# Performance work log

Measured on AMD Instinct MI355X. Metric: run time of the kernel, lower is better.

Reference implementation:

```python
import jax, jax.numpy as jnp
import numpy as np

N_NODES = 50000
N_EDGES = 600000
N_FEAT = 256
N_HID = 128
N_CLASS = 64
HEADS = 8
LEAKY_SLOPE = 0.2


def setup_inputs() -> dict:
    key = jax.random.key(0)
    ks = jax.random.split(key, 12)
    D0 = N_HID // HEADS  # 16 per-head dim, layer 0
    x = jax.random.normal(ks[0], (N_NODES, N_FEAT), dtype=jnp.float32)
    edge_index = jax.random.randint(ks[1], (2, N_EDGES), 0, N_NODES, dtype=jnp.int64)
    s0 = 1.0 / np.sqrt(N_FEAT)
    s1 = 1.0 / np.sqrt(N_HID)
    return {
        "x": x,
        "edge_index": edge_index,
        "W0": jax.random.normal(ks[2], (N_FEAT, HEADS * D0), dtype=jnp.float32) * s0,
        "a_src0": jax.random.normal(ks[3], (HEADS, D0), dtype=jnp.float32) * s0,
        "a_dst0": jax.random.normal(ks[4], (HEADS, D0), dtype=jnp.float32) * s0,
        "b0": jnp.zeros((HEADS * D0,), dtype=jnp.float32),
        "W1": jax.random.normal(ks[5], (N_HID, HEADS * N_CLASS), dtype=jnp.float32) * s1,
        "a_src1": jax.random.normal(ks[6], (HEADS, N_CLASS), dtype=jnp.float32) * s1,
        "a_dst1": jax.random.normal(ks[7], (HEADS, N_CLASS), dtype=jnp.float32) * s1,
        "b1": jnp.zeros((N_CLASS,), dtype=jnp.float32),
    }


def gat_conv(x, src, dst, W, a_s, a_d, b, concat, num_nodes):
    H, D = a_s.shape
    h = (x @ W).reshape(-1, H, D)                    # [N, H, D]
    alpha_s = jnp.einsum('nhd,hd->nh', h, a_s)       # [N, H]
    alpha_d = jnp.einsum('nhd,hd->nh', h, a_d)       # [N, H]
    e = jax.nn.leaky_relu(alpha_s[src] + alpha_d[dst], LEAKY_SLOPE)  # [E, H]
    # numerically stable edge-softmax grouped by destination node
    m = jax.ops.segment_max(e, dst, num_segments=num_nodes)
    m = jnp.where(jnp.isfinite(m), m, 0.0)           # nodes with no in-edges
    ex = jnp.exp(e - m[dst])
    denom = jax.ops.segment_sum(ex, dst, num_segments=num_nodes)
    alpha = ex / (denom[dst] + 1e-16)                # [E, H]
    msg = h[src] * alpha[:, :, None]                 # [E, H, D]
    out = jax.ops.segment_sum(msg, dst, num_segments=num_nodes)  # [N, H, D]
    if concat:
        out = out.reshape(num_nodes, H * D)
    else:
        out = out.mean(axis=1)
    return out + b


def reference(x, edge_index, W0, a_src0, a_dst0, b0, W1, a_src1, a_dst1, b1):
    src, dst = edge_index[0], edge_index[1]
    h = gat_conv(x, src, dst, W0, a_src0, a_dst0, b0, True, N_NODES)
    h = jax.nn.elu(h)  # eval mode: dropout is identity
    h = gat_conv(h, src, dst, W1, a_src1, a_dst1, b1, False, N_NODES)
    return jax.nn.log_softmax(h, axis=-1)
```

## Files before the change

### kernel.cpp

```cpp
#include <hip/hip_runtime.h>
#include <hip/hip_bf16.h>
#include <math.h>

#define NN 50000
#define NE 600000
#define NF 256
#define NHID 128
#define HEADS 8
#define D0 16
#define NCLS 64
#define NB1 196

#define PK0 (9 * 8 * 64 * 8)
#define PK1 (4 * 32 * 64 * 8)
#define PKA (4 * 64 * 8)
#define PREPN (PK0 + PK1 + PKA)

typedef __attribute__((ext_vector_type(8))) short short8;
typedef __attribute__((ext_vector_type(4))) float floatx4;

__device__ __forceinline__ float bf16lo(uint v) { return __uint_as_float((v & 0xffffu) << 16); }
__device__ __forceinline__ float bf16hi(uint v) { return __uint_as_float(v & 0xffff0000u); }
__device__ __forceinline__ uint packbf16(float a, float b) {
    return (uint)__bfloat16_as_ushort(__float2bfloat16(a)) |
           ((uint)__bfloat16_as_ushort(__float2bfloat16(b)) << 16);
}
__device__ __forceinline__ short f2bf(float v) {
    return (short)__bfloat16_as_ushort(__float2bfloat16(v));
}
__device__ __forceinline__ float bf16tof(short v) {
    return __uint_as_float(((uint)(ushort)v) << 16);
}


__global__ void scan1_kernel(const int* __restrict__ deg, int* __restrict__ rs,
                             int* __restrict__ bsum) {
    __shared__ int sh[256];
    int tid = threadIdx.x;
    int i = blockIdx.x * 256 + tid;
    int v = (i < NN) ? deg[i] : 0;
    sh[tid] = v;
    __syncthreads();
    for (int off = 1; off < 256; off <<= 1) {
        int t = (tid >= off) ? sh[tid - off] : 0;
        __syncthreads();
        sh[tid] += t;
        __syncthreads();
    }
    if (i < NN) rs[i] = sh[tid] - v;
    if (tid == 255) bsum[blockIdx.x] = sh[255];
}

__global__ void scan2_kernel(const int* __restrict__ bsum, int* __restrict__ bsumx) {
    __shared__ int sh[256];
    int tid = threadIdx.x;
    int v = (tid < NB1) ? bsum[tid] : 0;
    sh[tid] = v;
    __syncthreads();
    for (int off = 1; off < 256; off <<= 1) {
        int t = (tid >= off) ? sh[tid - off] : 0;
        __syncthreads();
        sh[tid] += t;
        __syncthreads();
    }
    if (tid < NB1) bsumx[tid] = sh[tid] - v;
}

__global__ void scan3_kernel(int* __restrict__ rs, const int* __restrict__ bsumx) {
    int i = blockIdx.x * 256 + threadIdx.x;
    if (i < NN) rs[i] += bsumx[i >> 8];
}

__global__ void scatter_kernel(const int* __restrict__ ei, const int* __restrict__ rs,
                               int* __restrict__ cnt2, int* __restrict__ csr) {
    int e = blockIdx.x * 256 + threadIdx.x;
    if (e >= NE) return;
    int s = ei[e], d = ei[NE + e];
    int pos = rs[d] + atomicAdd(&cnt2[d], 1);
    csr[pos] = s;
}


__global__ void fused_prep_kernel(const int* __restrict__ ei, int* __restrict__ deg,
                                  const float* __restrict__ W0, const float* __restrict__ aS0,
                                  const float* __restrict__ aD0, const float* __restrict__ W1,
                                  const float* __restrict__ aS1, const float* __restrict__ aD1,
                                  short* __restrict__ Bp0, short* __restrict__ Bp1,
                                  short* __restrict__ wA1b) {
    int e = blockIdx.x * 256 + threadIdx.x;
    if (e < NE) {
        atomicAdd(&deg[ei[NE + e]], 1);
        return;
    }
    int tid = e - NE;
    if (tid < PK0) {
        int j = tid & 7, l = (tid >> 3) & 63, ks = (tid >> 9) & 7, t = tid >> 12;
        int k = ks * 32 + (l >> 4) * 8 + j;
        float v;
        if (t < 8) {
            int c = t * 16 + (l & 15);
            v = W0[(size_t)k * 128 + c];
        } else {
            int jj = l & 15;
            int hh = jj & 7;
            const float* av = (jj < 8) ? aS0 : aD0;
            float sum = 0.f;
            for (int dd = 0; dd < D0; ++dd)
                sum += W0[(size_t)k * 128 + hh * D0 + dd] * av[hh * D0 + dd];
            v = sum;
        }
        Bp0[tid] = f2bf(v);
    } else if (tid < PK0 + PK1) {
        int t2 = tid - PK0;
        int j = t2 & 7, l = (t2 >> 3) & 63, ks = (t2 >> 9) & 31, t = t2 >> 14;
        int kk = ks * 32 + (l >> 4) * 8 + j;
        int c = t * 16 + (l & 15);
        Bp1[t2] = f2bf(W1[(size_t)(kk & 127) * 512 + (kk >> 7) * 64 + c] * 0.125f);
    } else if (tid < PREPN) {
        int t3 = tid - PK0 - PK1;
        int j = t3 & 7, l = (t3 >> 3) & 63, ks = t3 >> 9;
        int k = ks * 32 + (l >> 4) * 8 + j;
        int c = l & 15;
        int h = c & 7;
        const float* av = (c < 8) ? aS1 : aD1;
        float sum = 0.f;
        for (int d2 = 0; d2 < NCLS; ++d2)
            sum += W1[(size_t)k * 512 + h * NCLS + d2] * av[h * NCLS + d2];
        wA1b[t3] = f2bf(sum);
    }
}


__global__ __launch_bounds__(256) void gemm0_mfma(const float* __restrict__ x,
                                                  const short* __restrict__ Bp,
                                                  ushort* __restrict__ h0b,
                                                  float* __restrict__ as0,
                                                  float* __restrict__ ad0) {
    int lane = threadIdx.x & 63, wave = threadIdx.x >> 6;
    int rg = wave >> 1, cg = wave & 1;
    int q = lane >> 4, c16 = lane & 15;
    int row0 = blockIdx.x * 32 + rg * 16;
    int arow = row0 + c16;
    if (arow > NN - 1) arow = NN - 1;
    const float* ap = x + (size_t)arow * NF + q * 8;
    floatx4 acc[5] = {};
#pragma unroll
    for (int ks = 0; ks < 8; ++ks) {
        float4 va = *(const float4*)(ap + ks * 32);
        float4 vb = *(const float4*)(ap + ks * 32 + 4);
        short8 af;
        af[0] = f2bf(va.x); af[1] = f2bf(va.y); af[2] = f2bf(va.z); af[3] = f2bf(va.w);
        af[4] = f2bf(vb.x); af[5] = f2bf(vb.y); af[6] = f2bf(vb.z); af[7] = f2bf(vb.w);
#pragma unroll
        for (int tt = 0; tt < 4; ++tt) {
            int t = cg * 4 + tt;
            short8 bf = *(const short8*)(Bp + (((size_t)t * 8 + ks) * 64 + lane) * 8);
            acc[tt] = __builtin_amdgcn_mfma_f32_16x16x32_bf16(af, bf, acc[tt], 0, 0, 0);
        }
        if (cg) {
            short8 bf = *(const short8*)(Bp + (((size_t)8 * 8 + ks) * 64 + lane) * 8);
            acc[4] = __builtin_amdgcn_mfma_f32_16x16x32_bf16(af, bf, acc[4], 0, 0, 0);
        }
    }
#pragma unroll
    for (int r = 0; r < 4; ++r) {
        int grow = row0 + q * 4 + r;
        if (grow >= NN) continue;
#pragma unroll
        for (int tt = 0; tt < 4; ++tt)
            h0b[(size_t)grow * NHID + cg * 64 + tt * 16 + c16] =
                (ushort)f2bf(acc[tt][r]);
        if (cg) {
            float v = acc[4][r];
            if (c16 < 8) as0[grow * 8 + c16] = v;
            else         ad0[grow * 8 + (c16 - 8)] = v;
        }
    }
}

__global__ __launch_bounds__(256) void alpha1_mfma(const ushort* __restrict__ x1b,
                                                   const short* __restrict__ wA1b,
                                                   float* __restrict__ as1,
                                                   float* __restrict__ ad1) {
    int lane = threadIdx.x & 63, wave = threadIdx.x >> 6;
    int q = lane >> 4, c16 = lane & 15;
    int row0 = blockIdx.x * 64 + wave * 16;
    int arow = row0 + c16;
    if (arow > NN - 1) arow = NN - 1;
    const short* ap = (const short*)x1b + (size_t)arow * NHID + q * 8;
    floatx4 acc = {};
#pragma unroll
    for (int ks = 0; ks < 4; ++ks) {
        short8 af = *(const short8*)(ap + ks * 32);
        short8 bf = *(const short8*)(wA1b + (((size_t)ks) * 64 + lane) * 8);
        acc = __builtin_amdgcn_mfma_f32_16x16x32_bf16(af, bf, acc, 0, 0, 0);
    }
#pragma unroll
    for (int r = 0; r < 4; ++r) {
        int grow = row0 + q * 4 + r;
        if (grow >= NN) continue;
        float v = acc[r];
        if (c16 < 8) as1[grow * 8 + c16] = v;
        else         ad1[grow * 8 + (c16 - 8)] = v;
    }
}


__global__ __launch_bounds__(256) void fused_edge0(
    const int* __restrict__ rs, const int* __restrict__ deg, const int* __restrict__ csr,
    const ushort* __restrict__ h0b, const float* __restrict__ as0, const float* __restrict__ ad0,
    const float* __restrict__ b0, ushort* __restrict__ x1b) {
    int d = (blockIdx.x * 256 + threadIdx.x) >> 6;
    int lane = threadIdx.x & 63;
    if (d >= NN) return;
    int row = rs[d], dg = deg[d];
    int hl = lane & 7, g = lane >> 3;
    int hp = lane >> 3;
    float adv = ad0[d * 8 + hl];
    float den = 0.f;
    float2 acc = {0.f, 0.f};
    for (int base = 0; base < dg; base += 16) {
        int i0 = base + g, i1 = base + 8 + g;
        int s0 = (i0 < dg) ? csr[row + i0] : 0;
        int s1 = (i1 < dg) ? csr[row + i1] : 0;
        float ev0 = as0[s0 * 8 + hl] + adv;
        ev0 = ev0 > 0.f ? ev0 : 0.2f * ev0;
        float p0 = (i0 < dg) ? __expf(ev0) : 0.f;
        float ev1 = as0[s1 * 8 + hl] + adv;
        ev1 = ev1 > 0.f ? ev1 : 0.2f * ev1;
        float p1 = (i1 < dg) ? __expf(ev1) : 0.f;
        den += p0 + p1;
        uint vbuf[16];
#pragma unroll
        for (int g2 = 0; g2 < 8; ++g2) {
            int sg = __builtin_amdgcn_readlane(s0, g2 * 8);
            vbuf[g2] = *(const uint*)(h0b + (size_t)sg * NHID + 2 * lane);
        }
#pragma unroll
        for (int g2 = 0; g2 < 8; ++g2) {
            int sg = __builtin_amdgcn_readlane(s1, g2 * 8);
            vbuf[8 + g2] = *(const uint*)(h0b + (size_t)sg * NHID + 2 * lane);
        }
#pragma unroll
        for (int g2 = 0; g2 < 8; ++g2) {
            float ph = __shfl(p0, g2 * 8 + hp);
            acc.x += bf16lo(vbuf[g2]) * ph;
            acc.y += bf16hi(vbuf[g2]) * ph;
        }
#pragma unroll
        for (int g2 = 0; g2 < 8; ++g2) {
            float ph = __shfl(p1, g2 * 8 + hp);
            acc.x += bf16lo(vbuf[8 + g2]) * ph;
            acc.y += bf16hi(vbuf[8 + g2]) * ph;
        }
    }
    den += __shfl_xor(den, 8);
    den += __shfl_xor(den, 16);
    den += __shfl_xor(den, 32);
    float dh = __shfl(den, hp);
    float inv = 1.f / (dh + 1e-16f);
    float2 bb = ((const float2*)b0)[lane];
    float o0 = acc.x * inv + bb.x;
    float o1 = acc.y * inv + bb.y;
    o0 = o0 > 0.f ? o0 : expf(o0) - 1.f;
    o1 = o1 > 0.f ? o1 : expf(o1) - 1.f;
    *(uint*)(x1b + (size_t)d * NHID + 2 * lane) = packbf16(o0, o1);
}

__global__ __launch_bounds__(256) void fused_edge1(
    const int* __restrict__ rs, const int* __restrict__ deg, const int* __restrict__ csr,
    const ushort* __restrict__ x1b, const float* __restrict__ as1, const float* __restrict__ ad1,
    const short* __restrict__ Bp1, const float* __restrict__ b1, float* __restrict__ out) {
    __shared__ ushort aggNsh[8][1032];
    __shared__ float Csh[4][8][64];
    int wave = threadIdx.x >> 6;
    int lane = threadIdx.x & 63;
    int gw = blockIdx.x * 4 + wave;
    int dA = 2 * gw;
    int dB = dA + 1;
    int q = lane >> 4, c16 = lane & 15, h7 = lane & 7;
    int d_l = (lane >= 32) ? dB : dA;
    int row_l = rs[d_l], dg_l = deg[d_l];
    bool V = ((lane & 8) == 0) == (lane < 32);
    float adv = ad1[d_l * 8 + h7];
    int dgA = __shfl(dg_l, 0);
    int dgB = __shfl(dg_l, 32);
    int dgmax = dgA > dgB ? dgA : dgB;
    float den = 0.f;
    floatx4 acc[8] = {};
    for (int base = 0; base < dgmax; base += 16) {
        short8 af;
        int sarr[8];
#pragma unroll
        for (int j = 0; j < 8; ++j) {
            int idx = base + (q & 1) * 8 + j;
            int s = 0;
            if (idx < dg_l) s = csr[row_l + idx];
            sarr[j] = s;
            float ev = as1[s * 8 + h7] + adv;
            ev = ev > 0.f ? ev : 0.2f * ev;
            float p = __expf(ev);
            p = (idx < dg_l && V) ? p : 0.f;
            short pb = f2bf(p);
            af[j] = pb;
            den += bf16tof(pb);
        }
#pragma unroll
        for (int t = 0; t < 8; ++t) {
            short8 bv;
#pragma unroll
            for (int j = 0; j < 8; ++j)
                bv[j] = (short)x1b[(size_t)sarr[j] * NHID + t * 16 + c16];
            acc[t] = __builtin_amdgcn_mfma_f32_16x16x32_bf16(af, bv, acc[t], 0, 0, 0);
        }
    }
    den += __shfl_xor(den, 8);
    den += __shfl_xor(den, 16);
    int hbase = (q & 1) * 4;
    int lrow = wave * 2 + (lane >> 5);
#pragma unroll
    for (int r = 0; r < 4; ++r) {
        int hh = hbase + r;
        float dh = __shfl(den, (lane & 32) + hh);
        float inv = 1.f / (dh + 1e-16f);
#pragma unroll
        for (int t = 0; t < 8; ++t)
            aggNsh[lrow][hh * 128 + t * 16 + c16] = (ushort)f2bf(acc[t][r] * inv);
    }
    __syncthreads();
    {
        floatx4 acc2[4] = {};
        const short* abase = (const short*)&aggNsh[c16 & 7][0];
        int ks0 = wave * 8;
#pragma unroll
        for (int kk = 0; kk < 8; ++kk) {
            int ks = ks0 + kk;
            short8 af2 = *(const short8*)(abase + ks * 32 + q * 8);
#pragma unroll
            for (int t = 0; t < 4; ++t) {
                short8 bf = *(const short8*)(Bp1 + (((size_t)t * 32 + ks) * 64 + lane) * 8);
                acc2[t] = __builtin_amdgcn_mfma_f32_16x16x32_bf16(af2, bf, acc2[t], 0, 0, 0);
            }
        }
        if (q < 2) {
#pragma unroll
            for (int r = 0; r < 4; ++r)
#pragma unroll
                for (int t = 0; t < 4; ++t)
                    Csh[wave][q * 4 + r][t * 16 + c16] = acc2[t][r];
        }
    }
    __syncthreads();
    float z0 = 0.f, z1 = 0.f;
#pragma unroll
    for (int w2 = 0; w2 < 4; ++w2) {
        z0 += Csh[w2][wave * 2][lane];
        z1 += Csh[w2][wave * 2 + 1][lane];
    }
    float bb = b1[lane];
    z0 += bb;
    z1 += bb;
    float mx0 = z0, mx1 = z1;
#pragma unroll
    for (int x = 1; x < 64; x <<= 1) {
        mx0 = fmaxf(mx0, __shfl_xor(mx0, x));
        mx1 = fmaxf(mx1, __shfl_xor(mx1, x));
    }
    float s0 = expf(z0 - mx0), s1 = expf(z1 - mx1);
#pragma unroll
    for (int x = 1; x < 64; x <<= 1) {
        s0 += __shfl_xor(s0, x);
        s1 += __shfl_xor(s1, x);
    }
    float lse0 = mx0 + logf(s0);
    float lse1 = mx1 + logf(s1);
    out[(size_t)dA * NCLS + lane] = z0 - lse0;
    out[(size_t)dB * NCLS + lane] = z1 - lse1;
}


extern "C" void kernel_launch(void* const* d_in, const int* in_sizes, int n_in,
                              void* d_out, int out_size, void* d_ws, size_t ws_size,
                              hipStream_t stream) {
    const float* x   = (const float*)d_in[0];
    const int*   ei  = (const int*)d_in[1];
    const float* W0  = (const float*)d_in[2];
    const float* aS0 = (const float*)d_in[3];
    const float* aD0 = (const float*)d_in[4];
    const float* b0  = (const float*)d_in[5];
    const float* W1  = (const float*)d_in[6];
    const float* aS1 = (const float*)d_in[7];
    const float* aD1 = (const float*)d_in[8];
    const float* b1  = (const float*)d_in[9];
    float* out = (float*)d_out;

    char* ws = (char*)d_ws;
    ushort* x1b = (ushort*)ws; ws += (size_t)NN * NHID * 2;
    ushort* h0b = (ushort*)ws; ws += (size_t)NN * NHID * 2;
    float* as0  = (float*)ws; ws += (size_t)NN * HEADS * 4;
    float* ad0  = (float*)ws; ws += (size_t)NN * HEADS * 4;
    float* as1  = (float*)ws; ws += (size_t)NN * HEADS * 4;
    float* ad1  = (float*)ws; ws += (size_t)NN * HEADS * 4;
    short* Bp0  = (short*)ws; ws += (size_t)PK0 * 2;
    short* Bp1  = (short*)ws; ws += (size_t)PK1 * 2;
    short* wA1b = (short*)ws; ws += (size_t)PKA * 2;
    int* deg    = (int*)ws; ws += (size_t)NN * 4;
    int* cnt2   = (int*)ws; ws += (size_t)NN * 4;
    int* rs     = (int*)ws; ws += (size_t)NN * 4;
    int* bsum   = (int*)ws; ws += 256 * 4;
    int* bsumx  = (int*)ws; ws += 256 * 4;
    int* csr    = (int*)ws; ws += (size_t)NE * 4;

    const int FUSEDN = NE + PREPN;

    hipMemsetAsync(deg, 0, (size_t)2 * NN * 4, stream);
    fused_prep_kernel<<<(FUSEDN + 255) / 256, 256, 0, stream>>>(
        ei, deg, W0, aS0, aD0, W1, aS1, aD1, Bp0, Bp1, wA1b);

    scan1_kernel<<<NB1, 256, 0, stream>>>(deg, rs, bsum);
    scan2_kernel<<<1, 256, 0, stream>>>(bsum, bsumx);
    scan3_kernel<<<NB1, 256, 0, stream>>>(rs, bsumx);
    scatter_kernel<<<(NE + 255) / 256, 256, 0, stream>>>(ei, rs, cnt2, csr);

    gemm0_mfma<<<(NN + 31) / 32, 256, 0, stream>>>(x, Bp0, h0b, as0, ad0);
    fused_edge0<<<(NN + 3) / 4, 256, 0, stream>>>(rs, deg, csr, h0b, as0, ad0, b0, x1b);

    alpha1_mfma<<<(NN + 63) / 64, 256, 0, stream>>>(x1b, wA1b, as1, ad1);
    fused_edge1<<<NN / 8, 256, 0, stream>>>(rs, deg, csr, x1b, as1, ad1, Bp1, b1, out);
}
```

Baseline: 310.0 us.

## Stage gathered neighbor features through LDS with coalesced 16-byte loads

In the layer-1 edge kernel, each wave now loads the neighbor rows of x1b for a 16-edge chunk with coalesced short8 vector loads into a per-wave, XOR-swizzled LDS buffer. It then builds the MFMA B operands from LDS instead of doing scalar 2-byte global gathers. Shared memory is merged into one union buffer that also holds the aggregation and Csh staging regions. The aim is to cut the number of uncoalesced global transactions, at the cost of extra LDS traffic and possible LDS hazards between loop iterations, since there is no barrier between the rewrite and the reads.

```diff
diff --git a/kernel.cpp b/kernel.cpp
--- a/kernel.cpp
+++ b/kernel.cpp
@@ -15,6 +15,10 @@
 #define PK1 (4 * 32 * 64 * 8)
 #define PKA (4 * 64 * 8)
 #define PREPN (PK0 + PK1 + PKA)
+
+#define REG 4360
+#define AGG1 2072
+#define CSH0 3104
 
 typedef __attribute__((ext_vector_type(8))) short short8;
 typedef __attribute__((ext_vector_type(4))) float floatx4;
@@ -271,32 +275,48 @@
     const int* __restrict__ rs, const int* __restrict__ deg, const int* __restrict__ csr,
     const ushort* __restrict__ x1b, const float* __restrict__ as1, const float* __restrict__ ad1,
     const short* __restrict__ Bp1, const float* __restrict__ b1, float* __restrict__ out) {
-    __shared__ ushort aggNsh[8][1032];
-    __shared__ float Csh[4][8][64];
+    __shared__ ushort smem[4][REG];
     int wave = threadIdx.x >> 6;
     int lane = threadIdx.x & 63;
     int gw = blockIdx.x * 4 + wave;
     int dA = 2 * gw;
     int dB = dA + 1;
     int q = lane >> 4, c16 = lane & 15, h7 = lane & 7;
-    int d_l = (lane >= 32) ? dB : dA;
+    int hi = lane >> 5;
+    int d_l = hi ? dB : dA;
     int row_l = rs[d_l], dg_l = deg[d_l];
     bool V = ((lane & 8) == 0) == (lane < 32);
     float adv = ad1[d_l * 8 + h7];
     int dgA = __shfl(dg_l, 0);
     int dgB = __shfl(dg_l, 32);
     int dgmax = dgA > dgB ? dgA : dgB;
+    ushort* bufw = &smem[wave][0];
+    int xread = 2 * (q & 1) + 4 * hi;
+    int Rbase = (q & 1) * 8 + hi * 16;
     float den = 0.f;
     floatx4 acc[8] = {};
     for (int base = 0; base < dgmax; base += 16) {
+        int sl = (base + (lane & 15) < dg_l) ? csr[row_l + base + (lane & 15)] : 0;
+#pragma unroll
+        for (int i = 0; i < 8; ++i) {
+            int r0 = (i < 4) ? 4 * i : 16 + 4 * (i - 4);
+            int lr0 = (i < 4) ? 4 * i : 32 + 4 * (i - 4);
+            int sA = __builtin_amdgcn_readlane(sl, lr0);
+            int sB = __builtin_amdgcn_readlane(sl, lr0 + 1);
+            int sC = __builtin_amdgcn_readlane(sl, lr0 + 2);
+            int sD = __builtin_amdgcn_readlane(sl, lr0 + 3);
+            int sub = lane >> 4;
+            int sg = sub == 0 ? sA : sub == 1 ? sB : sub == 2 ? sC : sD;
+            short8 v = *(const short8*)(x1b + (size_t)sg * NHID + c16 * 8);
+            int xr = 2 * (r0 >> 3);
+            *(short8*)(bufw + (r0 + sub) * 136 + ((c16 ^ xr) * 8)) = v;
+        }
         short8 af;
-        int sarr[8];
 #pragma unroll
         for (int j = 0; j < 8; ++j) {
             int idx = base + (q & 1) * 8 + j;
             int s = 0;
             if (idx < dg_l) s = csr[row_l + idx];
-            sarr[j] = s;
             float ev = as1[s * 8 + h7] + adv;
             ev = ev > 0.f ? ev : 0.2f * ev;
             float p = __expf(ev);
@@ -307,17 +327,17 @@
         }
 #pragma unroll
         for (int t = 0; t < 8; ++t) {
+            int sp = (2 * t + (c16 >> 3)) ^ xread;
             short8 bv;
 #pragma unroll
             for (int j = 0; j < 8; ++j)
-                bv[j] = (short)x1b[(size_t)sarr[j] * NHID + t * 16 + c16];
+                bv[j] = (short)bufw[(Rbase + j) * 136 + sp * 8 + (c16 & 7)];
             acc[t] = __builtin_amdgcn_mfma_f32_16x16x32_bf16(af, bv, acc[t], 0, 0, 0);
         }
     }
     den += __shfl_xor(den, 8);
     den += __shfl_xor(den, 16);
     int hbase = (q & 1) * 4;
-    int lrow = wave * 2 + (lane >> 5);
 #pragma unroll
     for (int r = 0; r < 4; ++r) {
         int hh = hbase + r;
@@ -325,12 +345,14 @@
         float inv = 1.f / (dh + 1e-16f);
 #pragma unroll
         for (int t = 0; t < 8; ++t)
-            aggNsh[lrow][hh * 128 + t * 16 + c16] = (ushort)f2bf(acc[t][r] * inv);
+            smem[wave][hi * AGG1 + hh * 128 + t * 16 + c16] =
+                (ushort)f2bf(acc[t][r] * inv);
     }
     __syncthreads();
     {
         floatx4 acc2[4] = {};
-        const short* abase = (const short*)&aggNsh[c16 & 7][0];
+        int ar = c16 & 7;
+        const ushort* abase = &smem[ar >> 1][(ar & 1) * AGG1];
         int ks0 = wave * 8;
 #pragma unroll
         for (int kk = 0; kk < 8; ++kk) {
@@ -343,19 +365,21 @@
             }
         }
         if (q < 2) {
+            float* csh = (float*)&smem[wave][CSH0];
 #pragma unroll
             for (int r = 0; r < 4; ++r)
 #pragma unroll
                 for (int t = 0; t < 4; ++t)
-                    Csh[wave][q * 4 + r][t * 16 + c16] = acc2[t][r];
+                    csh[(q * 4 + r) * 64 + t * 16 + c16] = acc2[t][r];
         }
     }
     __syncthreads();
     float z0 = 0.f, z1 = 0.f;
 #pragma unroll
     for (int w2 = 0; w2 < 4; ++w2) {
-        z0 += Csh[w2][wave * 2][lane];
-        z1 += Csh[w2][wave * 2 + 1][lane];
+        const float* csh = (const float*)&smem[w2][CSH0];
+        z0 += csh[(wave * 2) * 64 + lane];
+        z1 += csh[(wave * 2 + 1) * 64 + lane];
     }
     float bb = b1[lane];
     z0 += bb;
```

Measured after the change: 310.3 us. No clear change (+0.1%).
